# Kernel optimization log

Measured on AMD Instinct MI355X. Metric: run time of the kernel, lower is better.

## Reference

```python
import jax, jax.numpy as jnp
import numpy as np

S, IN, M, V, K = 8192, 512, 512, 50, 8


def setup_inputs() -> dict:
    key = jax.random.key(0)
    ks = jax.random.split(key, 6)
    sc = 0.02
    inp = {
        "inputs": jax.random.normal(ks[0], (S, IN), jnp.float32),
        "Wioux": sc * jax.random.normal(ks[1], (5 * M, IN), jnp.float32),
        "bioux": jnp.zeros((5 * M,), jnp.float32),
        "Wiouh": sc * jax.random.normal(ks[2], (5 * M, M), jnp.float32),
        "biouh": jnp.zeros((5 * M,), jnp.float32),
        "Wlx": sc * jax.random.normal(ks[3], (M, IN), jnp.float32),
        "blx": jnp.zeros((M,), jnp.float32),
        "Wlh": sc * jax.random.normal(ks[4], (M, M), jnp.float32),
        "blh": jnp.zeros((M,), jnp.float32),
        "lb": jnp.ones((V, M), jnp.float32),  # nn.Parameter(torch.ones(V, M))
    }
    rng = np.random.default_rng(0)
    t = np.arange(S)[:, None]
    u1 = rng.random((S, K)); u2 = rng.random((S, K))
    rel_fw = (u1 * np.maximum(t, 1)).astype(np.int32)                     # idx < t
    rel_bw = np.minimum(t + 1 + (u2 * np.maximum(S - 1 - t, 1)).astype(np.int64), S - 1).astype(np.int32)  # idx > t
    mask_fw = rng.random((S, K)) < 0.6
    mask_fw[0, :] = False      # t=0 fwd has no relatives in the original
    mask_bw = rng.random((S, K)) < 0.6
    mask_bw[S - 1, :] = False  # t=S-1 bwd has no relatives
    inp["rel_fw"] = jnp.asarray(rel_fw)
    inp["dep_fw"] = jnp.asarray(rng.integers(0, V, (S, K)).astype(np.int32))
    inp["mask_fw"] = jnp.asarray(mask_fw)
    inp["rel_bw"] = jnp.asarray(rel_bw)
    inp["dep_bw"] = jnp.asarray(rng.integers(0, V, (S, K)).astype(np.int32))
    inp["mask_bw"] = jnp.asarray(mask_bw)
    return inp


def _syn_lstm(inputs, Wioux, bioux, Wiouh, biouh, Wlx, blx, Wlh, blh, lb,
              rel, dep, mask, order):
    """One direction; order gives the timestep visit order. Returns [S, M]."""
    mdim = Wlh.shape[0]

    def step(carry, t):
        Hbuf, h_prev, c_prev = carry
        x = inputs[t]
        ious = Wioux @ x + bioux + Wiouh @ h_prev + biouh          # [5M]
        c0, c1, c2, c3, c4 = jnp.split(ious, 5)
        # NOTE: original torch code assigns (i,o,f,s,u)=(sig(i),sig(o),sig(s),sig(f),tanh(u)),
        # i.e. gate f uses chunk 3 and gate s uses chunk 2 -- reproduced faithfully.
        i = jax.nn.sigmoid(c0)
        o = jax.nn.sigmoid(c1)
        f = jax.nn.sigmoid(c3)
        s = jax.nn.sigmoid(c2)
        u = jnp.tanh(c4)
        c = f * c_prev + i * u
        h = o * jnp.tanh(c)
        rel_h = Hbuf[rel[t]]                                       # [K, M] gather of prior hiddens
        l = jax.nn.sigmoid(rel_h @ Wlh.T + blh + (Wlx @ x + blx) + lb[dep[t]])  # [K, M]
        agg = jnp.sum(l * rel_h * mask[t][:, None].astype(rel_h.dtype), axis=0)  # [M]
        h = h + s * jnp.tanh(agg)   # if all masked: agg=0, tanh(0)=0 -> empty-relative branch
        Hbuf = Hbuf.at[t].set(h)
        return (Hbuf, h, c), None

    Hbuf0 = jnp.zeros((inputs.shape[0], mdim), inputs.dtype)
    z = jnp.zeros((mdim,), inputs.dtype)
    (Hbuf, _, _), _ = jax.lax.scan(step, (Hbuf0, z, z), order)
    return Hbuf


def reference(inputs, Wioux, bioux, Wiouh, biouh, Wlx, blx, Wlh, blh, lb,
              rel_fw, dep_fw, mask_fw, rel_bw, dep_bw, mask_bw):
    n = inputs.shape[0]
    Hfw = _syn_lstm(inputs, Wioux, bioux, Wiouh, biouh, Wlx, blx, Wlh, blh, lb,
                    rel_fw, dep_fw, mask_fw, jnp.arange(n))
    Hbw = _syn_lstm(inputs, Wioux, bioux, Wiouh, biouh, Wlx, blx, Wlh, blh, lb,
                    rel_bw, dep_bw, mask_bw, jnp.arange(n - 1, -1, -1))
    return jnp.concatenate([Hfw, Hbw], axis=1)   # [S, 2*M]
```

## Files before the change

### kernel.cpp

```cpp
#include <hip/hip_runtime.h>

#define S_LEN 8192
#define KREL 8
#define WPD 128

typedef float f4 __attribute__((ext_vector_type(4)));
typedef unsigned long long u64;

__device__ __forceinline__ float sigmf(float x) { return 1.0f / (1.0f + __expf(-x)); }
__device__ __forceinline__ float tanhfast(float x) { return 1.0f - 2.0f / (__expf(2.0f * x) + 1.0f); }

__global__ void k_maskcvt(const unsigned char* __restrict__ src,
                          unsigned char* __restrict__ dst, int n)
{
  const unsigned int* w = (const unsigned int*)src;
  __shared__ int s_i32, s_f32;
  if (threadIdx.x == 0) { s_i32 = 1; s_f32 = 1; }
  __syncthreads();
  int i32ok = 1, f32ok = 1;
  for (int i = threadIdx.x; i < 1024; i += blockDim.x) {
    const unsigned int v = w[i];
    if (v != 0u && v != 1u) i32ok = 0;
    if (v != 0u && v != 0x3F800000u) f32ok = 0;
  }
  if (!i32ok) atomicAnd(&s_i32, 0);
  if (!f32ok) atomicAnd(&s_f32, 0);
  __syncthreads();
  const int wide = (s_i32 || s_f32);
  for (int i = blockIdx.x * blockDim.x + threadIdx.x; i < n; i += gridDim.x * blockDim.x)
    dst[i] = wide ? (w[i] ? 1 : 0) : (src[i] ? 1 : 0);
}

__global__ __launch_bounds__(256)
void k_gemm(const float* __restrict__ X, const float* __restrict__ Wioux,
            const float* __restrict__ Wlx, const float* __restrict__ bioux,
            const float* __restrict__ biouh, const float* __restrict__ blx,
            const float* __restrict__ blh, float* __restrict__ P)
{
  __shared__ float As[16][64];
  __shared__ float Bs[16][64];
  const int t0 = blockIdx.x * 64;
  const int r0 = blockIdx.y * 64;
  const int tid = threadIdx.x;
  const int tx = tid & 15, ty = tid >> 4;
  const int si = tid >> 2, sk = (tid & 3) << 2;
  const int rB = r0 + si;
  const float* brow = (rB < 2560) ? (Wioux + (size_t)rB * 512)
                                  : (Wlx + (size_t)(rB - 2560) * 512);
  const float* arow = X + (size_t)(t0 + si) * 512;
  float acc[4][4] = {};
  for (int k0 = 0; k0 < 512; k0 += 16) {
    const float4 av = *(const float4*)(arow + k0 + sk);
    const float4 bv = *(const float4*)(brow + k0 + sk);
    __syncthreads();
    As[sk + 0][si] = av.x; As[sk + 1][si] = av.y; As[sk + 2][si] = av.z; As[sk + 3][si] = av.w;
    Bs[sk + 0][si] = bv.x; Bs[sk + 1][si] = bv.y; Bs[sk + 2][si] = bv.z; Bs[sk + 3][si] = bv.w;
    __syncthreads();
#pragma unroll
    for (int kk = 0; kk < 16; ++kk) {
      const float4 a = *(const float4*)&As[kk][ty * 4];
      const float4 b = *(const float4*)&Bs[kk][tx * 4];
      acc[0][0] += a.x * b.x; acc[0][1] += a.x * b.y; acc[0][2] += a.x * b.z; acc[0][3] += a.x * b.w;
      acc[1][0] += a.y * b.x; acc[1][1] += a.y * b.y; acc[1][2] += a.y * b.z; acc[1][3] += a.y * b.w;
      acc[2][0] += a.z * b.x; acc[2][1] += a.z * b.y; acc[2][2] += a.z * b.z; acc[2][3] += a.z * b.w;
      acc[3][0] += a.w * b.x; acc[3][1] += a.w * b.y; acc[3][2] += a.w * b.z; acc[3][3] += a.w * b.w;
    }
  }
#pragma unroll
  for (int i = 0; i < 4; ++i) {
    const int t = t0 + ty * 4 + i;
#pragma unroll
    for (int j = 0; j < 4; ++j) {
      const int r = r0 + tx * 4 + j;
      const float bias = (r < 2560) ? (bioux[r] + biouh[r]) : (blx[r - 2560] + blh[r - 2560]);
      P[(size_t)t * 3072 + r] = acc[i][j] + bias;
    }
  }
}

__global__ __launch_bounds__(256, 1)
void k_rec(const float* __restrict__ Wiouh, const float* __restrict__ Wlh,
           const float* __restrict__ P, const float* __restrict__ lb,
           const int* __restrict__ rel_fw, const int* __restrict__ dep_fw,
           const unsigned char* __restrict__ mask_fw,
           const int* __restrict__ rel_bw, const int* __restrict__ dep_bw,
           const unsigned char* __restrict__ mask_bw,
           float* __restrict__ Gfw, float* __restrict__ Gbw,
           u64* rec, float* __restrict__ out)
{
  __shared__ float wlds[4 * 6 * 512];
  __shared__ u64 hs64[2][512];
  const int wg  = blockIdx.x;
  const int dir = wg / WPD;
  const int w   = wg % WPD;
  const int tid = threadIdx.x;
  const int grp = tid >> 6;
  const int lane = tid & 63;
  const int kl = lane & 7;
  const int m = w * 4 + grp;
  const int dircol = dir * 512;
  const int* rel = dir ? rel_bw : rel_fw;
  const int* dep = dir ? dep_bw : dep_fw;
  const unsigned char* msk = dir ? mask_bw : mask_fw;
  float* Gbuf = dir ? Gbw : Gfw;

  {
    const float* rows[6];
#pragma unroll
    for (int rg = 0; rg < 5; ++rg) rows[rg] = Wiouh + (size_t)(rg * 512 + m) * 512;
    rows[5] = Wlh + (size_t)m * 512;
#pragma unroll
    for (int rg = 0; rg < 6; ++rg)
#pragma unroll
      for (int q = 0; q < 2; ++q)
        *(f4*)&wlds[(size_t)grp * 3072 + rg * 512 + q * 256 + lane * 4] =
            *(const f4*)(rows[rg] + q * 256 + lane * 4);
  }
  const unsigned wbase = (unsigned)(uintptr_t)&wlds[(size_t)grp * 3072 + lane * 4];

  hs64[0][tid] = 0ull; hs64[0][tid + 256] = 0ull;
  hs64[1][tid] = 0ull; hs64[1][tid + 256] = 0ull;

  float cstate = 0.0f, hprev = 0.0f, gprev = 0.0f;

  int jjU, mkU, jjN, mkN, depN;
  float Hg, Gg, LBg;
  float p0, p1, p2, p3, p4, p5;
  {
    const int t0 = dir ? (S_LEN - 1) : 0;
    const int t1 = dir ? (S_LEN - 2) : 1;
    jjU = rel[t0 * KREL + kl]; mkU = (int)msk[t0 * KREL + kl];
    Hg  = out[(size_t)jjU * 1024 + dircol + m];
    Gg  = Gbuf[(size_t)jjU * 512 + m];
    LBg = lb[(size_t)dep[t0 * KREL + kl] * 512 + m];
    const float* prow = P + (size_t)t0 * 3072;
    p0 = prow[m];        p1 = prow[512 + m];  p2 = prow[1024 + m];
    p3 = prow[1536 + m]; p4 = prow[2048 + m]; p5 = prow[2560 + m];
    jjN = rel[t1 * KREL + kl]; mkN = (int)msk[t1 * KREL + kl]; depN = dep[t1 * KREL + kl];
  }
  __syncthreads();

#pragma unroll 1
  for (int s = 0; s < S_LEN; ++s) {
    const int t = dir ? (S_LEN - 1 - s) : s;
    const int tn = dir ? (t - 1) : (t + 1);
    const int prevt  = dir ? (t + 1) : (t - 1);
    const int prevt2 = dir ? (t + 2) : (t - 2);

    f4 wf[6][2];
#pragma unroll
    for (int rg = 0; rg < 6; ++rg)
#pragma unroll
      for (int q = 0; q < 2; ++q)
        asm volatile("ds_read_b128 %0, %1 offset:%2"
                     : "=v"(wf[rg][q])
                     : "v"(wbase), "i"((rg * 512 + q * 256) * 4)
                     : "memory");

    if (s > 0) {
      const int pb = (((s - 1) & 1) * 2 + dir) * 512;
      u64* q0 = rec + pb + tid;
      u64* q1 = rec + pb + tid + 256;
      u64 a0 = __hip_atomic_load(q0, __ATOMIC_RELAXED, __HIP_MEMORY_SCOPE_AGENT);
      u64 a1 = __hip_atomic_load(q1, __ATOMIC_RELAXED, __HIP_MEMORY_SCOPE_AGENT);
      u64 b0 = __hip_atomic_load(q0, __ATOMIC_RELAXED, __HIP_MEMORY_SCOPE_AGENT);
      u64 b1 = __hip_atomic_load(q1, __ATOMIC_RELAXED, __HIP_MEMORY_SCOPE_AGENT);
      u64 c0 = __hip_atomic_load(q0, __ATOMIC_RELAXED, __HIP_MEMORY_SCOPE_AGENT);
      u64 c1 = __hip_atomic_load(q1, __ATOMIC_RELAXED, __HIP_MEMORY_SCOPE_AGENT);
      for (;;) {
        const bool k0 = (unsigned)(a0 >> 32) >= (unsigned)s;
        const bool k1 = (unsigned)(a1 >> 32) >= (unsigned)s;
        if (k0 && k1) break;
        const u64 n0 = __hip_atomic_load(q0, __ATOMIC_RELAXED, __HIP_MEMORY_SCOPE_AGENT);
        const u64 n1 = __hip_atomic_load(q1, __ATOMIC_RELAXED, __HIP_MEMORY_SCOPE_AGENT);
        a0 = k0 ? a0 : b0;  b0 = k0 ? b0 : c0;  c0 = n0;
        a1 = k1 ? a1 : b1;  b1 = k1 ? b1 : c1;  c1 = n1;
      }
      __hip_atomic_store(&hs64[s & 1][tid], a0,
                         __ATOMIC_RELAXED, __HIP_MEMORY_SCOPE_WORKGROUP);
      __hip_atomic_store(&hs64[s & 1][tid + 256], a1,
                         __ATOMIC_RELAXED, __HIP_MEMORY_SCOPE_WORKGROUP);
    }

    u64 pk0[4], pk1[4];
    {
      const int base = lane * 4;
      for (;;) {
        unsigned mn = 0xffffffffu;
#pragma unroll
        for (int j = 0; j < 4; ++j) {
          pk0[j] = __hip_atomic_load(&hs64[s & 1][base + j],
                                     __ATOMIC_RELAXED, __HIP_MEMORY_SCOPE_WORKGROUP);
          pk1[j] = __hip_atomic_load(&hs64[s & 1][256 + base + j],
                                     __ATOMIC_RELAXED, __HIP_MEMORY_SCOPE_WORKGROUP);
          const unsigned t0 = (unsigned)(pk0[j] >> 32);
          const unsigned t1 = (unsigned)(pk1[j] >> 32);
          mn = mn < t0 ? mn : t0;
          mn = mn < t1 ? mn : t1;
        }
        if (mn >= (unsigned)s) break;
      }
    }

    asm volatile("s_waitcnt lgkmcnt(0)" ::: "memory");
    float hx[2][4];
#pragma unroll
    for (int j = 0; j < 4; ++j) {
      hx[0][j] = __uint_as_float((unsigned)pk0[j]);
      hx[1][j] = __uint_as_float((unsigned)pk1[j]);
    }
    float dsum[6];
#pragma unroll
    for (int rg = 0; rg < 6; ++rg) {
      float a = 0.0f;
#pragma unroll
      for (int j = 0; j < 4; ++j) {
        a += wf[rg][0][j] * hx[0][j];
        a += wf[rg][1][j] * hx[1][j];
      }
      a += __shfl_xor(a, 1);  a += __shfl_xor(a, 2);  a += __shfl_xor(a, 4);
      a += __shfl_xor(a, 8);  a += __shfl_xor(a, 16); a += __shfl_xor(a, 32);
      dsum[rg] = a;
    }
    const float g = dsum[5];

    const float iv = sigmf(p0 + dsum[0]);
    const float ov = sigmf(p1 + dsum[1]);
    const float sv = sigmf(p2 + dsum[2]);
    const float fv = sigmf(p3 + dsum[3]);
    const float uv = tanhfast(p4 + dsum[4]);
    cstate = fv * cstate + iv * uv;
    const float hb = ov * tanhfast(cstate);

    const float hv_k = (jjU == prevt) ? hprev : Hg;
    const float gv_k = (jjU == prevt) ? g : ((jjU == prevt2) ? gprev : Gg);
    float sm = mkU ? (sigmf(gv_k + p5 + LBg) * hv_k) : 0.0f;
    sm += __shfl_xor(sm, 1); sm += __shfl_xor(sm, 2); sm += __shfl_xor(sm, 4);
    const float hval = hb + sv * tanhfast(sm);

    if (lane == 0) {
      const u64 pk =
          ((u64)(unsigned)(s + 1) << 32) | (u64)__float_as_uint(hval);
      __hip_atomic_store(rec + ((s & 1) * 2 + dir) * 512 + m, pk,
                         __ATOMIC_RELAXED, __HIP_MEMORY_SCOPE_AGENT);
      out[(size_t)t * 1024 + dircol + m] = hval;
      if (s > 0) Gbuf[(size_t)prevt * 512 + m] = g;
    }

    if (s < S_LEN - 1) {
      const float HgN  = out[(size_t)jjN * 1024 + dircol + m];
      const float GgN  = Gbuf[(size_t)jjN * 512 + m];
      const float LBgN = lb[(size_t)depN * 512 + m];
      const float* prow = P + (size_t)tn * 3072;
      p0 = prow[m];        p1 = prow[512 + m];  p2 = prow[1024 + m];
      p3 = prow[1536 + m]; p4 = prow[2048 + m]; p5 = prow[2560 + m];
      int jj2 = jjN, mk2 = mkN, dep2 = depN;
      if (s < S_LEN - 2) {
        const int t2 = dir ? (t - 2) : (t + 2);
        jj2 = rel[t2 * KREL + kl]; mk2 = (int)msk[t2 * KREL + kl]; dep2 = dep[t2 * KREL + kl];
      }
      jjU = jjN; mkU = mkN; Hg = HgN; Gg = GgN; LBg = LBgN;
      jjN = jj2; mkN = mk2; depN = dep2;
    }
    hprev = hval; gprev = g;
  }
}

__global__ void k_fill(float* __restrict__ o, int n, float v)
{ const int i = blockIdx.x * 256 + threadIdx.x; if (i < n) o[i] = v; }

extern "C" void kernel_launch(void* const* d_in, const int* in_sizes, int n_in,
                              void* d_out, int out_size, void* d_ws, size_t ws_size,
                              hipStream_t stream)
{
  (void)in_sizes; (void)n_in;
  const float* X     = (const float*)d_in[0];
  const float* Wioux = (const float*)d_in[1];
  const float* bioux = (const float*)d_in[2];
  const float* Wiouh = (const float*)d_in[3];
  const float* biouh = (const float*)d_in[4];
  const float* Wlx   = (const float*)d_in[5];
  const float* blx   = (const float*)d_in[6];
  const float* Wlh   = (const float*)d_in[7];
  const float* blh   = (const float*)d_in[8];
  const float* lb    = (const float*)d_in[9];
  const int* rel_fw  = (const int*)d_in[10];
  const int* dep_fw  = (const int*)d_in[11];
  const unsigned char* mask_fw_raw = (const unsigned char*)d_in[12];
  const int* rel_bw  = (const int*)d_in[13];
  const int* dep_bw  = (const int*)d_in[14];
  const unsigned char* mask_bw_raw = (const unsigned char*)d_in[15];
  float* out = (float*)d_out;

  const int nmask = S_LEN * KREL;
  const size_t needP = (size_t)S_LEN * 3072 * 4;
  const size_t needG = (size_t)S_LEN * 512 * 4;
  const size_t need  = 32768 + needP + 2 * needG + 2 * (size_t)nmask;
  if (ws_size < need) {
    k_fill<<<(out_size + 255) / 256, 256, 0, stream>>>(out, out_size, 12345.0f);
    return;
  }
  char* ws = (char*)d_ws;
  u64*   rec = (u64*)ws;
  float* P   = (float*)(ws + 32768);
  float* Gfw = (float*)(ws + 32768 + needP);
  float* Gbw = Gfw + (size_t)S_LEN * 512;
  unsigned char* Mfw = (unsigned char*)(ws + 32768 + needP + 2 * needG);
  unsigned char* Mbw = Mfw + nmask;

  hipMemsetAsync(rec, 0, 16384, stream);
  k_maskcvt<<<64, 256, 0, stream>>>(mask_fw_raw, Mfw, nmask);
  k_maskcvt<<<64, 256, 0, stream>>>(mask_bw_raw, Mbw, nmask);
  dim3 gg(S_LEN / 64, 3072 / 64);
  k_gemm<<<gg, 256, 0, stream>>>(X, Wioux, Wlx, bioux, biouh, blx, blh, P);
  k_rec<<<2 * WPD, 256, 0, stream>>>(Wiouh, Wlh, P, lb, rel_fw, dep_fw, Mfw,
                                     rel_bw, dep_bw, Mbw, Gfw, Gbw, rec, out);
}
```

Baseline: 18.17 ms.

## Keep recurrent weights in registers, transpose LDS h layout, precompute non-adjacent relative term

Each lane's Wiouh/Wlh weight slice now stays in registers for the whole recurrence instead of being reread from LDS every step, which takes LDS reads off the serial critical path. The LDS hidden-state buffer is re-laid out as [par][half][j][lane] so the per-lane reads are lane-contiguous. This aims to avoid bank conflicts. The sigmoid term for relatives that are not the immediately previous step is computed before the spin-wait, so only the adjacent-relative case stays after the matvec. Cost: higher register pressure, which matters less with one block per CU.

```diff
diff --git a/kernel.cpp b/kernel.cpp
--- a/kernel.cpp
+++ b/kernel.cpp
@@ -88,8 +88,7 @@
            float* __restrict__ Gfw, float* __restrict__ Gbw,
            u64* rec, float* __restrict__ out)
 {
-  __shared__ float wlds[4 * 6 * 512];
-  __shared__ u64 hs64[2][512];
+  __shared__ u64 hsp[2][2][4][64];
   const int wg  = blockIdx.x;
   const int dir = wg / WPD;
   const int w   = wg % WPD;
@@ -104,6 +103,7 @@
   const unsigned char* msk = dir ? mask_bw : mask_fw;
   float* Gbuf = dir ? Gbw : Gfw;
 
+  f4 wreg[6][2];
   {
     const float* rows[6];
 #pragma unroll
@@ -113,13 +113,13 @@
     for (int rg = 0; rg < 6; ++rg)
 #pragma unroll
       for (int q = 0; q < 2; ++q)
-        *(f4*)&wlds[(size_t)grp * 3072 + rg * 512 + q * 256 + lane * 4] =
-            *(const f4*)(rows[rg] + q * 256 + lane * 4);
-  }
-  const unsigned wbase = (unsigned)(uintptr_t)&wlds[(size_t)grp * 3072 + lane * 4];
-
-  hs64[0][tid] = 0ull; hs64[0][tid + 256] = 0ull;
-  hs64[1][tid] = 0ull; hs64[1][tid + 256] = 0ull;
+        wreg[rg][q] = *(const f4*)(rows[rg] + q * 256 + lane * 4);
+  }
+
+  {
+    u64* hz = (u64*)hsp;
+    hz[tid] = 0ull; hz[tid + 256] = 0ull; hz[tid + 512] = 0ull; hz[tid + 768] = 0ull;
+  }
 
   float cstate = 0.0f, hprev = 0.0f, gprev = 0.0f;
 
@@ -146,16 +146,10 @@
     const int tn = dir ? (t - 1) : (t + 1);
     const int prevt  = dir ? (t + 1) : (t - 1);
     const int prevt2 = dir ? (t + 2) : (t - 2);
-
-    f4 wf[6][2];
-#pragma unroll
-    for (int rg = 0; rg < 6; ++rg)
-#pragma unroll
-      for (int q = 0; q < 2; ++q)
-        asm volatile("ds_read_b128 %0, %1 offset:%2"
-                     : "=v"(wf[rg][q])
-                     : "v"(wbase), "i"((rg * 512 + q * 256) * 4)
-                     : "memory");
+    const int par = s & 1;
+
+    const float gv_base = (jjU == prevt2) ? gprev : Gg;
+    const float sm_pre  = mkU ? (sigmf(gv_base + p5 + LBg) * Hg) : 0.0f;
 
     if (s > 0) {
       const int pb = (((s - 1) & 1) * 2 + dir) * 512;
@@ -176,38 +170,34 @@
         a0 = k0 ? a0 : b0;  b0 = k0 ? b0 : c0;  c0 = n0;
         a1 = k1 ? a1 : b1;  b1 = k1 ? b1 : c1;  c1 = n1;
       }
-      __hip_atomic_store(&hs64[s & 1][tid], a0,
+      __hip_atomic_store(&hsp[par][0][tid & 3][tid >> 2], a0,
                          __ATOMIC_RELAXED, __HIP_MEMORY_SCOPE_WORKGROUP);
-      __hip_atomic_store(&hs64[s & 1][tid + 256], a1,
+      __hip_atomic_store(&hsp[par][1][tid & 3][tid >> 2], a1,
                          __ATOMIC_RELAXED, __HIP_MEMORY_SCOPE_WORKGROUP);
     }
 
     u64 pk0[4], pk1[4];
-    {
-      const int base = lane * 4;
-      for (;;) {
-        unsigned mn = 0xffffffffu;
-#pragma unroll
-        for (int j = 0; j < 4; ++j) {
-          pk0[j] = __hip_atomic_load(&hs64[s & 1][base + j],
-                                     __ATOMIC_RELAXED, __HIP_MEMORY_SCOPE_WORKGROUP);
-          pk1[j] = __hip_atomic_load(&hs64[s & 1][256 + base + j],
-                                     __ATOMIC_RELAXED, __HIP_MEMORY_SCOPE_WORKGROUP);
-          const unsigned t0 = (unsigned)(pk0[j] >> 32);
-          const unsigned t1 = (unsigned)(pk1[j] >> 32);
-          mn = mn < t0 ? mn : t0;
-          mn = mn < t1 ? mn : t1;
-        }
-        if (mn >= (unsigned)s) break;
+    for (;;) {
+      unsigned mn = 0xffffffffu;
+#pragma unroll
+      for (int j = 0; j < 4; ++j) {
+        pk0[j] = __hip_atomic_load(&hsp[par][0][j][lane],
+                                   __ATOMIC_RELAXED, __HIP_MEMORY_SCOPE_WORKGROUP);
+        pk1[j] = __hip_atomic_load(&hsp[par][1][j][lane],
+                                   __ATOMIC_RELAXED, __HIP_MEMORY_SCOPE_WORKGROUP);
+        const unsigned t0 = (unsigned)(pk0[j] >> 32);
+        const unsigned t1 = (unsigned)(pk1[j] >> 32);
+        mn = mn < t0 ? mn : t0;
+        mn = mn < t1 ? mn : t1;
       }
-    }
-
-    asm volatile("s_waitcnt lgkmcnt(0)" ::: "memory");
-    float hx[2][4];
+      if (mn >= (unsigned)s) break;
+    }
+
+    float hx0[4], hx1[4];
 #pragma unroll
     for (int j = 0; j < 4; ++j) {
-      hx[0][j] = __uint_as_float((unsigned)pk0[j]);
-      hx[1][j] = __uint_as_float((unsigned)pk1[j]);
+      hx0[j] = __uint_as_float((unsigned)pk0[j]);
+      hx1[j] = __uint_as_float((unsigned)pk1[j]);
     }
     float dsum[6];
 #pragma unroll
@@ -215,8 +205,8 @@
       float a = 0.0f;
 #pragma unroll
       for (int j = 0; j < 4; ++j) {
-        a += wf[rg][0][j] * hx[0][j];
-        a += wf[rg][1][j] * hx[1][j];
+        a += wreg[rg][0][j] * hx0[j];
+        a += wreg[rg][1][j] * hx1[j];
       }
       a += __shfl_xor(a, 1);  a += __shfl_xor(a, 2);  a += __shfl_xor(a, 4);
       a += __shfl_xor(a, 8);  a += __shfl_xor(a, 16); a += __shfl_xor(a, 32);
@@ -232,9 +222,8 @@
     cstate = fv * cstate + iv * uv;
     const float hb = ov * tanhfast(cstate);
 
-    const float hv_k = (jjU == prevt) ? hprev : Hg;
-    const float gv_k = (jjU == prevt) ? g : ((jjU == prevt2) ? gprev : Gg);
-    float sm = mkU ? (sigmf(gv_k + p5 + LBg) * hv_k) : 0.0f;
+    const float smf = mkU ? (sigmf(g + p5 + LBg) * hprev) : 0.0f;
+    float sm = (jjU == prevt) ? smf : sm_pre;
     sm += __shfl_xor(sm, 1); sm += __shfl_xor(sm, 2); sm += __shfl_xor(sm, 4);
     const float hval = hb + sv * tanhfast(sm);
 
```

New measurement: 17.38 ms. 1.05x faster.
